# Kernel tuning notes

Measured on AMD Instinct MI355X. Metric: run time of the kernel, lower is better.

The kernel has to match this reference:

```python
import jax, jax.numpy as jnp
import numpy as np

B, L, H = 32, 1024, 384


def setup_inputs() -> dict:
    key = jax.random.key(0)
    k1, k2 = jax.random.split(key)
    encoder_hidden_states = jax.random.normal(k1, (B, L, H), dtype=jnp.float32)
    durations_gt = jax.random.randint(k2, (B, L), 0, 8, dtype=jnp.int32)
    return {"encoder_hidden_states": encoder_hidden_states, "durations_gt": durations_gt}


def reference(encoder_hidden_states, durations_gt):
    # cumulative end-frame of each phoneme: [B, L]
    cum = jnp.cumsum(durations_gt, axis=1)
    total = cum[:, -1]                      # [B] expanded length per batch item
    T = int(jnp.max(total))                 # max expanded length (data-dependent)
    t = jnp.arange(T, dtype=cum.dtype)      # [T] output frame positions
    # source phoneme index for each output frame: number of cum entries <= t
    idx = jax.vmap(lambda c: jnp.searchsorted(c, t, side="right"))(cum)  # [B, T]
    idx = jnp.minimum(idx, L - 1)
    mask = (t[None, :] < total[:, None]).astype(jnp.float32)             # [B, T]
    # gather hidden states and zero out the padded tail
    out = jnp.take_along_axis(encoder_hidden_states, idx[:, :, None], axis=1)
    out = out * mask[:, :, None]
    return out, mask
```

## Files before the change

kernel.cpp:

```cpp
#include <hip/hip_runtime.h>

#define BB 32
#define LL 1024
#define HH 384
#define H4 (HH / 4)
#define TT 64
#define NT 256

__global__ __launch_bounds__(NT) void lenreg_kernel(
    const float* __restrict__ ehs,
    const int* __restrict__ dur,
    float* __restrict__ out,
    float* __restrict__ mask,
    int T)
{
    __shared__ int scum[LL];
    __shared__ int psum[NT];
    __shared__ int sidx[TT];

    const int tid = threadIdx.x;
    const int b   = blockIdx.y;
    const int t0  = blockIdx.x * TT;

    int4 d = ((const int4*)(dur + (size_t)b * LL))[tid];
    int p0 = d.x;
    int p1 = p0 + d.y;
    int p2 = p1 + d.z;
    int p3 = p2 + d.w;
    psum[tid] = p3;
    __syncthreads();
    #pragma unroll
    for (int off = 1; off < NT; off <<= 1) {
        int v = (tid >= off) ? psum[tid - off] : 0;
        __syncthreads();
        psum[tid] += v;
        __syncthreads();
    }
    const int excl = (tid > 0) ? psum[tid - 1] : 0;
    scum[4 * tid + 0] = excl + p0;
    scum[4 * tid + 1] = excl + p1;
    scum[4 * tid + 2] = excl + p2;
    scum[4 * tid + 3] = excl + p3;
    __syncthreads();

    const int total = scum[LL - 1];

    if (tid < TT) {
        const int t = t0 + tid;
        int lo = 0, hi = LL;
        while (lo < hi) {
            const int mid = (lo + hi) >> 1;
            if (scum[mid] <= t) lo = mid + 1; else hi = mid;
        }
        sidx[tid] = (lo < LL - 1) ? lo : (LL - 1);
        if (t < T) mask[(size_t)b * T + t] = (t < total) ? 1.0f : 0.0f;
    }
    __syncthreads();

    const float4* __restrict__ src_base = (const float4*)(ehs + (size_t)b * LL * HH);
    float4* __restrict__ out4 = (float4*)out;
    const float4 zero4 = make_float4(0.f, 0.f, 0.f, 0.f);

    for (int w = tid; w < TT * H4; w += NT) {
        const int tl = w / H4;
        const int v  = w - tl * H4;
        const int t  = t0 + tl;
        if (t >= T) break;
        float4 val = zero4;
        if (t < total) {
            val = src_base[(size_t)sidx[tl] * H4 + v];
        }
        out4[((size_t)b * T + t) * H4 + v] = val;
    }
}

extern "C" void kernel_launch(void* const* d_in, const int* in_sizes, int n_in,
                              void* d_out, int out_size, void* d_ws, size_t ws_size,
                              hipStream_t stream) {
    const float* ehs = (const float*)d_in[0];
    const int*   dur = (const int*)d_in[1];

    const int T = out_size / (BB * (HH + 1));

    float* out  = (float*)d_out;
    float* mask = (float*)d_out + (size_t)BB * T * HH;

    dim3 grid((T + TT - 1) / TT, BB);
    dim3 block(NT);
    lenreg_kernel<<<grid, block, 0, stream>>>(ehs, dur, out, mask, T);
}
```

Baseline: 230.5 us.

## Split into prefix-sum expand kernel plus gather kernel using workspace index map

Adds a per-batch kernel that computes the duration prefix sum once, writes a source index for every output frame into workspace, and writes the mask. A second kernel then gathers rows using that index map with a fully unrolled main loop. This removes the redundant prefix scan and binary search that every tile block repeated in the fused kernel. The cost is an extra launch and a global round trip for the index buffer, and the expand kernel runs on only one block per batch with serial per-thread fill loops. The fused kernel stays as a fallback when workspace is too small.

Measured after the change: 237.4 us. 3.0% more time.

```diff
diff --git a/kernel.cpp b/kernel.cpp
--- a/kernel.cpp
+++ b/kernel.cpp
@@ -6,6 +6,89 @@
 #define H4 (HH / 4)
 #define TT 64
 #define NT 256
+
+__global__ __launch_bounds__(NT) void expand_kernel(
+    const int* __restrict__ dur,
+    int* __restrict__ srcidx,
+    float* __restrict__ mask,
+    int T)
+{
+    __shared__ int psum[NT];
+
+    const int tid = threadIdx.x;
+    const int b   = blockIdx.x;
+
+    int4 d = ((const int4*)(dur + (size_t)b * LL))[tid];
+    int p0 = d.x;
+    int p1 = p0 + d.y;
+    int p2 = p1 + d.z;
+    int p3 = p2 + d.w;
+    psum[tid] = p3;
+    __syncthreads();
+    #pragma unroll
+    for (int off = 1; off < NT; off <<= 1) {
+        int v = (tid >= off) ? psum[tid - off] : 0;
+        __syncthreads();
+        psum[tid] += v;
+        __syncthreads();
+    }
+    const int excl  = (tid > 0) ? psum[tid - 1] : 0;
+    const int total = psum[NT - 1];
+
+    int* __restrict__ sb = srcidx + (size_t)b * T;
+    const int e0 = excl + p0;
+    const int e1 = excl + p1;
+    const int e2 = excl + p2;
+    const int e3 = excl + p3;
+    const int l0 = 4 * tid;
+    for (int k = excl; k < e0; ++k) sb[k] = l0 + 0;
+    for (int k = e0;   k < e1; ++k) sb[k] = l0 + 1;
+    for (int k = e1;   k < e2; ++k) sb[k] = l0 + 2;
+    for (int k = e2;   k < e3; ++k) sb[k] = l0 + 3;
+
+    for (int t = total + tid; t < T; t += NT) sb[t] = -1;
+
+    float* __restrict__ mb = mask + (size_t)b * T;
+    for (int t = tid; t < T; t += NT) mb[t] = (t < total) ? 1.0f : 0.0f;
+}
+
+__global__ __launch_bounds__(NT) void gather_kernel(
+    const float* __restrict__ ehs,
+    const int* __restrict__ srcidx,
+    float* __restrict__ out,
+    int T)
+{
+    const int b  = blockIdx.y;
+    const int t0 = blockIdx.x * TT;
+
+    const float4* __restrict__ src = (const float4*)(ehs + (size_t)b * LL * HH);
+    float4* __restrict__ ob        = (float4*)out + ((size_t)b * T + t0) * (size_t)H4;
+    const int* __restrict__ sb     = srcidx + (size_t)b * T + t0;
+    const float4 zero4 = make_float4(0.f, 0.f, 0.f, 0.f);
+
+    if (t0 + TT <= T) {
+        #pragma unroll
+        for (int i = 0; i < (TT * H4) / NT; ++i) {
+            const int w   = threadIdx.x + i * NT;
+            const int tl  = w / H4;
+            const int v   = w - tl * H4;
+            const int idx = sb[tl];
+            float4 val = zero4;
+            if (idx >= 0) val = src[(size_t)idx * H4 + v];
+            ob[w] = val;
+        }
+    } else {
+        const int wmax = (T - t0) * H4;
+        for (int w = threadIdx.x; w < wmax; w += NT) {
+            const int tl  = w / H4;
+            const int v   = w - tl * H4;
+            const int idx = sb[tl];
+            float4 val = zero4;
+            if (idx >= 0) val = src[(size_t)idx * H4 + v];
+            ob[w] = val;
+        }
+    }
+}
 
 __global__ __launch_bounds__(NT) void lenreg_kernel(
     const float* __restrict__ ehs,
@@ -85,7 +168,15 @@
     float* out  = (float*)d_out;
     float* mask = (float*)d_out + (size_t)BB * T * HH;
 
+    const size_t need = (size_t)BB * (size_t)T * sizeof(int);
     dim3 grid((T + TT - 1) / TT, BB);
     dim3 block(NT);
-    lenreg_kernel<<<grid, block, 0, stream>>>(ehs, dur, out, mask, T);
+
+    if (d_ws != nullptr && ws_size >= need) {
+        int* srcidx = (int*)d_ws;
+        expand_kernel<<<dim3(BB), block, 0, stream>>>(dur, srcidx, mask, T);
+        gather_kernel<<<grid, block, 0, stream>>>(ehs, srcidx, out, T);
+    } else {
+        lenreg_kernel<<<grid, block, 0, stream>>>(ehs, dur, out, mask, T);
+    }
 }
```

## Use wave-shuffle scan, branchless search, unrolled fast path and nontemporal stores

Applied to the files above, without the earlier changes.

Replaces the shared-memory Hillis-Steele prefix sum with a wavefront shuffle scan plus a small cross-wave combine, which removes many block barriers. The binary search becomes a fixed-step branchless search. Fully valid tiles take an unrolled copy path that preloads the row indices into registers so several loads can be in flight. Output writes use nontemporal stores to avoid polluting the cache, at some cost in code size and branching.

Result: no change. 227.6 us, median of 2 (-1.2%).

```diff
diff --git a/kernel.cpp b/kernel.cpp
--- a/kernel.cpp
+++ b/kernel.cpp
@@ -6,6 +6,10 @@
 #define H4 (HH / 4)
 #define TT 64
 #define NT 256
+#define NW (NT / 64)
+#define WPT (TT * H4 / NT)
+
+typedef float f4 __attribute__((ext_vector_type(4)));
 
 __global__ __launch_bounds__(NT) void lenreg_kernel(
     const float* __restrict__ ehs,
@@ -15,62 +19,87 @@
     int T)
 {
     __shared__ int scum[LL];
-    __shared__ int psum[NT];
+    __shared__ int wsum[NW];
     __shared__ int sidx[TT];
 
-    const int tid = threadIdx.x;
-    const int b   = blockIdx.y;
-    const int t0  = blockIdx.x * TT;
+    const int tid  = threadIdx.x;
+    const int lane = tid & 63;
+    const int wid  = tid >> 6;
+    const int b    = blockIdx.y;
+    const int t0   = blockIdx.x * TT;
 
     int4 d = ((const int4*)(dur + (size_t)b * LL))[tid];
-    int p0 = d.x;
-    int p1 = p0 + d.y;
-    int p2 = p1 + d.z;
-    int p3 = p2 + d.w;
-    psum[tid] = p3;
+    const int p0 = d.x;
+    const int p1 = p0 + d.y;
+    const int p2 = p1 + d.z;
+    const int p3 = p2 + d.w;
+
+    int v = p3;
+    #pragma unroll
+    for (int off = 1; off < 64; off <<= 1) {
+        const int n = __shfl_up(v, off, 64);
+        if (lane >= off) v += n;
+    }
+    if (lane == 63) wsum[wid] = v;
     __syncthreads();
+
+    int woff = 0, total = 0;
     #pragma unroll
-    for (int off = 1; off < NT; off <<= 1) {
-        int v = (tid >= off) ? psum[tid - off] : 0;
-        __syncthreads();
-        psum[tid] += v;
-        __syncthreads();
+    for (int w = 0; w < NW; ++w) {
+        const int s = wsum[w];
+        woff  += (w < wid) ? s : 0;
+        total += s;
     }
-    const int excl = (tid > 0) ? psum[tid - 1] : 0;
+
+    const int excl = woff + v - p3;
     scum[4 * tid + 0] = excl + p0;
     scum[4 * tid + 1] = excl + p1;
     scum[4 * tid + 2] = excl + p2;
     scum[4 * tid + 3] = excl + p3;
     __syncthreads();
 
-    const int total = scum[LL - 1];
-
     if (tid < TT) {
         const int t = t0 + tid;
-        int lo = 0, hi = LL;
-        while (lo < hi) {
-            const int mid = (lo + hi) >> 1;
-            if (scum[mid] <= t) lo = mid + 1; else hi = mid;
+        int pos = 0;
+        #pragma unroll
+        for (int step = LL / 2; step > 0; step >>= 1) {
+            if (scum[pos + step - 1] <= t) pos += step;
         }
-        sidx[tid] = (lo < LL - 1) ? lo : (LL - 1);
+        sidx[tid] = (pos < LL - 1) ? pos : (LL - 1);
         if (t < T) mask[(size_t)b * T + t] = (t < total) ? 1.0f : 0.0f;
     }
     __syncthreads();
 
-    const float4* __restrict__ src_base = (const float4*)(ehs + (size_t)b * LL * HH);
-    float4* __restrict__ out4 = (float4*)out;
-    const float4 zero4 = make_float4(0.f, 0.f, 0.f, 0.f);
+    const f4* __restrict__ src = (const f4*)(ehs + (size_t)b * LL * HH);
+    f4* __restrict__ ob = (f4*)out + ((size_t)b * T + t0) * (size_t)H4;
 
-    for (int w = tid; w < TT * H4; w += NT) {
-        const int tl = w / H4;
-        const int v  = w - tl * H4;
-        const int t  = t0 + tl;
-        if (t >= T) break;
-        float4 val = zero4;
-        if (t < total) {
-            val = src_base[(size_t)sidx[tl] * H4 + v];
+    const int tlim = (T < total) ? T : total;
+    if (t0 + TT <= tlim) {
+        int idxr[WPT];
+        #pragma unroll
+        for (int i = 0; i < WPT; ++i) {
+            idxr[i] = sidx[(tid + i * NT) / H4];
         }
-        out4[((size_t)b * T + t) * H4 + v] = val;
+        #pragma unroll
+        for (int i = 0; i < WPT; ++i) {
+            const int w  = tid + i * NT;
+            const int tl = w / H4;
+            const int vv = w - tl * H4;
+            const f4 val = src[(size_t)idxr[i] * H4 + vv];
+            __builtin_nontemporal_store(val, &ob[w]);
+        }
+    } else {
+        const int tend = (T < t0 + TT) ? T : (t0 + TT);
+        const int wmax = (tend > t0) ? (tend - t0) * H4 : 0;
+        const f4 zero4 = (f4){0.f, 0.f, 0.f, 0.f};
+        for (int w = tid; w < wmax; w += NT) {
+            const int tl = w / H4;
+            const int vv = w - tl * H4;
+            const int t  = t0 + tl;
+            f4 val = zero4;
+            if (t < total) val = src[(size_t)sidx[tl] * H4 + vv];
+            __builtin_nontemporal_store(val, &ob[w]);
+        }
     }
 }
 
```
